# Performance work log

Measured on AMD Instinct MI355X. Metric: run time of the kernel, lower is better.

## Reference

```python
import jax, jax.numpy as jnp
import numpy as np


def setup_inputs() -> dict:
    key = jax.random.key(0)
    k1, k2 = jax.random.split(key)
    N, K, D = 65536, 512, 512
    x = jax.random.normal(k1, (N, D), dtype=jnp.float32)
    centroids = jax.random.normal(k2, (K, D), dtype=jnp.float32)
    return {"x": x, "centroids": centroids}


def reference(x, centroids):
    # Squared pairwise distances via matmul expansion (same math as
    # sum((x[:,None,:] - c[None,:,:])**2, axis=2), without the [N,K,D] blowup):
    x_sq = jnp.sum(x * x, axis=1, keepdims=True)            # [N, 1]
    c_sq = jnp.sum(centroids * centroids, axis=1)            # [K]
    d2 = x_sq + c_sq[None, :] - 2.0 * (x @ centroids.T)      # [N, K]
    q = 1.0 / (1.0 + d2)                                     # Student-t kernel, alpha=1
    q = q / jnp.sum(q, axis=1, keepdims=True)                # row normalize
    return q
```

## Files before the change

kernel.cpp:

```cpp
#include <hip/hip_runtime.h>
#include <stdint.h>


#define D 512
#define K 512
#define BM 64
#define BK 64
#define NCHUNK (D / BK)
#define THREADS 512

typedef __attribute__((ext_vector_type(8))) short short8;
typedef __attribute__((ext_vector_type(4))) float floatx4;

__device__ __forceinline__ uint16_t f2bf(float f) {
  uint32_t u = __float_as_uint(f);
  u += 0x7FFFu + ((u >> 16) & 1u);
  return (uint16_t)(u >> 16);
}

__global__ __launch_bounds__(64)
void prep_kernel(const float* __restrict__ cent, float* __restrict__ csq,
                 uint16_t* __restrict__ bbf) {
  const int row  = blockIdx.x;
  const int lane = threadIdx.x;
  const float4* src = (const float4*)(cent + (size_t)row * D + lane * 8);
  float4 v0 = src[0];
  float4 v1 = src[1];
  float ss = v0.x*v0.x + v0.y*v0.y + v0.z*v0.z + v0.w*v0.w
           + v1.x*v1.x + v1.y*v1.y + v1.z*v1.z + v1.w*v1.w;
  uint4 pk;
  pk.x = (uint32_t)f2bf(v0.x) | ((uint32_t)f2bf(v0.y) << 16);
  pk.y = (uint32_t)f2bf(v0.z) | ((uint32_t)f2bf(v0.w) << 16);
  pk.z = (uint32_t)f2bf(v1.x) | ((uint32_t)f2bf(v1.y) << 16);
  pk.w = (uint32_t)f2bf(v1.z) | ((uint32_t)f2bf(v1.w) << 16);
  const int c = lane >> 3;
  const int g = lane & 7;
  const int slot = (c * K + row) * 8 + (g ^ (row & 7));
  *(uint4*)(bbf + (size_t)slot * 8) = pk;
  #pragma unroll
  for (int m = 1; m < 64; m <<= 1) ss += __shfl_xor(ss, m);
  if (lane == 0) csq[row] = ss;
}

__global__ __launch_bounds__(THREADS, 4)
void cluster_main(const float* __restrict__ x, const uint16_t* __restrict__ bbf,
                  const float* __restrict__ csq, float* __restrict__ out) {
  __shared__ __align__(16) uint16_t lA[BM * BK];
  __shared__ __align__(16) uint16_t lB[K * BK];
  __shared__ float lcsq[K];
  __shared__ float lxsq[BM];
  __shared__ float lrow[BM];

  const int tid  = threadIdx.x;
  const int wave = tid >> 6;
  const int lane = tid & 63;
  const int p    = lane & 15;
  const int quad = lane >> 4;
  const int row0 = blockIdx.x * BM;

  lcsq[tid] = csq[tid];
  if (tid < BM) { lxsq[tid] = 0.f; lrow[tid] = 0.f; }

  const int ar = tid >> 3;
  const int ag = tid & 7;
  const float* aptr = x + (size_t)(row0 + ar) * D + ag * 8;
  uint16_t* adst = &lA[(size_t)(ar * 8 + (ag ^ (ar & 7))) * 8];
  float xacc = 0.f;

  floatx4 acc[4][4];
  #pragma unroll
  for (int mi = 0; mi < 4; ++mi)
    #pragma unroll
    for (int ni = 0; ni < 4; ++ni)
      acc[mi][ni] = (floatx4){0.f, 0.f, 0.f, 0.f};

  for (int c = 0; c < NCHUNK; ++c) {
    __syncthreads();

    float4 v0 = *(const float4*)(aptr);
    float4 v1 = *(const float4*)(aptr + 4);
    aptr += BK;
    xacc += v0.x*v0.x + v0.y*v0.y + v0.z*v0.z + v0.w*v0.w
          + v1.x*v1.x + v1.y*v1.y + v1.z*v1.z + v1.w*v1.w;
    uint4 pk;
    pk.x = (uint32_t)f2bf(v0.x) | ((uint32_t)f2bf(v0.y) << 16);
    pk.y = (uint32_t)f2bf(v0.z) | ((uint32_t)f2bf(v0.w) << 16);
    pk.z = (uint32_t)f2bf(v1.x) | ((uint32_t)f2bf(v1.y) << 16);
    pk.w = (uint32_t)f2bf(v1.z) | ((uint32_t)f2bf(v1.w) << 16);
    *(uint4*)adst = pk;

    {
      const uint16_t* bsrc = bbf + (size_t)c * (K * BK) + wave * 4096 + lane * 8;
      #pragma unroll
      for (int j = 0; j < 8; ++j) {
        __builtin_amdgcn_global_load_lds(
            (const __attribute__((address_space(1))) uint32_t*)(bsrc + j * 512),
            (__attribute__((address_space(3))) uint32_t*)(&lB[wave * 4096 + j * 512]),
            16, 0, 0);
      }
    }

    __syncthreads();

    #pragma unroll
    for (int kk = 0; kk < 2; ++kk) {
      short8 af[4], bfr[4];
      #pragma unroll
      for (int mi = 0; mi < 4; ++mi) {
        const int r = mi * 16 + p;
        const int g = (kk * 4 + quad) ^ (r & 7);
        af[mi] = *(const short8*)&lA[(size_t)(r * 8 + g) * 8];
      }
      #pragma unroll
      for (int ni = 0; ni < 4; ++ni) {
        const int r = wave * 64 + ni * 16 + p;
        const int g = (kk * 4 + quad) ^ (r & 7);
        bfr[ni] = *(const short8*)&lB[(size_t)(r * 8 + g) * 8];
      }
      #pragma unroll
      for (int mi = 0; mi < 4; ++mi)
        #pragma unroll
        for (int ni = 0; ni < 4; ++ni)
          acc[mi][ni] = __builtin_amdgcn_mfma_f32_16x16x32_bf16(
              af[mi], bfr[ni], acc[mi][ni], 0, 0, 0);
    }
  }

  atomicAdd(&lxsq[ar], xacc);
  __syncthreads();

  float xs[4][4];
  #pragma unroll
  for (int mi = 0; mi < 4; ++mi)
    #pragma unroll
    for (int rr = 0; rr < 4; ++rr)
      xs[mi][rr] = lxsq[mi * 16 + quad * 4 + rr];
  float cs[4];
  #pragma unroll
  for (int ni = 0; ni < 4; ++ni)
    cs[ni] = lcsq[wave * 64 + ni * 16 + p];

  float rp[4][4];
  #pragma unroll
  for (int mi = 0; mi < 4; ++mi)
    #pragma unroll
    for (int rr = 0; rr < 4; ++rr)
      rp[mi][rr] = 0.f;

  #pragma unroll
  for (int mi = 0; mi < 4; ++mi)
    #pragma unroll
    for (int ni = 0; ni < 4; ++ni)
      #pragma unroll
      for (int rr = 0; rr < 4; ++rr) {
        const float d = 1.0f + xs[mi][rr] + cs[ni] - 2.0f * acc[mi][ni][rr];
        const float q = __builtin_amdgcn_rcpf(d);
        acc[mi][ni][rr] = q;
        rp[mi][rr] += q;
      }

  #pragma unroll
  for (int mi = 0; mi < 4; ++mi)
    #pragma unroll
    for (int rr = 0; rr < 4; ++rr) {
      float v = rp[mi][rr];
      v += __shfl_xor(v, 1);
      v += __shfl_xor(v, 2);
      v += __shfl_xor(v, 4);
      v += __shfl_xor(v, 8);
      if (p == 0) atomicAdd(&lrow[mi * 16 + quad * 4 + rr], v);
    }
  __syncthreads();

  #pragma unroll
  for (int mi = 0; mi < 4; ++mi) {
    #pragma unroll
    for (int rr = 0; rr < 4; ++rr) {
      const int row = mi * 16 + quad * 4 + rr;
      const float inv = __builtin_amdgcn_rcpf(lrow[row]);
      float* orow = out + (size_t)(row0 + row) * K + wave * 64 + p;
      #pragma unroll
      for (int ni = 0; ni < 4; ++ni)
        orow[ni * 16] = acc[mi][ni][rr] * inv;
    }
  }
}

extern "C" void kernel_launch(void* const* d_in, const int* in_sizes, int n_in,
                              void* d_out, int out_size, void* d_ws, size_t ws_size,
                              hipStream_t stream) {
  const float* x    = (const float*)d_in[0];
  const float* cent = (const float*)d_in[1];
  float* out = (float*)d_out;

  float*    csq = (float*)d_ws;
  uint16_t* bbf = (uint16_t*)((char*)d_ws + 2048);

  const int N = in_sizes[0] / D;
  prep_kernel<<<K, 64, 0, stream>>>(cent, csq, bbf);
  cluster_main<<<N / BM, THREADS, 0, stream>>>(x, bbf, csq, out);
}
```

Baseline: 260.7 us.

## Double-buffer LDS tiles with halved K-chunk and register prefetch of x

```diff
diff --git a/kernel.cpp b/kernel.cpp
--- a/kernel.cpp
+++ b/kernel.cpp
@@ -5,7 +5,7 @@
 #define D 512
 #define K 512
 #define BM 64
-#define BK 64
+#define BK 32
 #define NCHUNK (D / BK)
 #define THREADS 512
 
@@ -16,6 +16,13 @@
   uint32_t u = __float_as_uint(f);
   u += 0x7FFFu + ((u >> 16) & 1u);
   return (uint16_t)(u >> 16);
+}
+
+__device__ __forceinline__ uint2 pack4(float4 v) {
+  uint2 p;
+  p.x = (uint32_t)f2bf(v.x) | ((uint32_t)f2bf(v.y) << 16);
+  p.y = (uint32_t)f2bf(v.z) | ((uint32_t)f2bf(v.w) << 16);
+  return p;
 }
 
 __global__ __launch_bounds__(64)
@@ -29,14 +36,11 @@
   float ss = v0.x*v0.x + v0.y*v0.y + v0.z*v0.z + v0.w*v0.w
            + v1.x*v1.x + v1.y*v1.y + v1.z*v1.z + v1.w*v1.w;
   uint4 pk;
-  pk.x = (uint32_t)f2bf(v0.x) | ((uint32_t)f2bf(v0.y) << 16);
-  pk.y = (uint32_t)f2bf(v0.z) | ((uint32_t)f2bf(v0.w) << 16);
-  pk.z = (uint32_t)f2bf(v1.x) | ((uint32_t)f2bf(v1.y) << 16);
-  pk.w = (uint32_t)f2bf(v1.z) | ((uint32_t)f2bf(v1.w) << 16);
-  const int c = lane >> 3;
-  const int g = lane & 7;
-  const int slot = (c * K + row) * 8 + (g ^ (row & 7));
-  *(uint4*)(bbf + (size_t)slot * 8) = pk;
+  { uint2 a = pack4(v0), b = pack4(v1); pk.x = a.x; pk.y = a.y; pk.z = b.x; pk.w = b.y; }
+  const int c = lane >> 2;
+  const int g = lane & 3;
+  const size_t eo = ((size_t)(c * K + row)) * 32 + (size_t)((g ^ ((row >> 2) & 3))) * 8;
+  *(uint4*)(bbf + eo) = pk;
   #pragma unroll
   for (int m = 1; m < 64; m <<= 1) ss += __shfl_xor(ss, m);
   if (lane == 0) csq[row] = ss;
@@ -45,8 +49,8 @@
 __global__ __launch_bounds__(THREADS, 4)
 void cluster_main(const float* __restrict__ x, const uint16_t* __restrict__ bbf,
                   const float* __restrict__ csq, float* __restrict__ out) {
-  __shared__ __align__(16) uint16_t lA[BM * BK];
-  __shared__ __align__(16) uint16_t lB[K * BK];
+  __shared__ __align__(16) uint16_t lA[2][BM * BK];
+  __shared__ __align__(16) uint16_t lB[2][K * BK];
   __shared__ float lcsq[K];
   __shared__ float lxsq[BM];
   __shared__ float lrow[BM];
@@ -56,16 +60,18 @@
   const int lane = tid & 63;
   const int p    = lane & 15;
   const int quad = lane >> 4;
+  const int sw   = quad ^ (p >> 2);
   const int row0 = blockIdx.x * BM;
 
   lcsq[tid] = csq[tid];
   if (tid < BM) { lxsq[tid] = 0.f; lrow[tid] = 0.f; }
 
-  const int ar = tid >> 3;
-  const int ag = tid & 7;
-  const float* aptr = x + (size_t)(row0 + ar) * D + ag * 8;
-  uint16_t* adst = &lA[(size_t)(ar * 8 + (ag ^ (ar & 7))) * 8];
-  float xacc = 0.f;
+  const int ar  = tid >> 3;
+  const int sub = tid & 7;
+  const int aidx = (ar * 4 + ((sub >> 1) ^ ((ar >> 2) & 3))) * 8 + (sub & 1) * 4;
+  const float* aptr = x + (size_t)(row0 + ar) * D + sub * 4;
+
+  const int bofs = wave * 2048 + lane * 8;
 
   floatx4 acc[4][4];
   #pragma unroll
@@ -74,55 +80,73 @@
     for (int ni = 0; ni < 4; ++ni)
       acc[mi][ni] = (floatx4){0.f, 0.f, 0.f, 0.f};
 
+  float xacc;
+  float4 areg;
+
+  {
+    const uint16_t* src = bbf + bofs;
+    uint16_t* dst = &lB[0][wave * 2048];
+    #pragma unroll
+    for (int j = 0; j < 4; ++j)
+      __builtin_amdgcn_global_load_lds(
+          (const __attribute__((address_space(1))) uint32_t*)(src + j * 512),
+          (__attribute__((address_space(3))) uint32_t*)(dst + j * 512),
+          16, 0, 0);
+    float4 a0 = *(const float4*)(aptr);
+    xacc = a0.x*a0.x + a0.y*a0.y + a0.z*a0.z + a0.w*a0.w;
+    *(uint2*)&lA[0][aidx] = pack4(a0);
+    areg = *(const float4*)(aptr + BK);
+  }
+  __syncthreads();
+  {
+    const uint16_t* src = bbf + (size_t)1 * (K * BK) + bofs;
+    uint16_t* dst = &lB[1][wave * 2048];
+    #pragma unroll
+    for (int j = 0; j < 4; ++j)
+      __builtin_amdgcn_global_load_lds(
+          (const __attribute__((address_space(1))) uint32_t*)(src + j * 512),
+          (__attribute__((address_space(3))) uint32_t*)(dst + j * 512),
+          16, 0, 0);
+  }
+
   for (int c = 0; c < NCHUNK; ++c) {
+    const int buf = c & 1;
+
+    if (c + 1 < NCHUNK) {
+      xacc += areg.x*areg.x + areg.y*areg.y + areg.z*areg.z + areg.w*areg.w;
+      *(uint2*)&lA[(c + 1) & 1][aidx] = pack4(areg);
+    }
+    if (c + 2 < NCHUNK) areg = *(const float4*)(aptr + (c + 2) * BK);
+
+    short8 af[4], bfr[4];
+    #pragma unroll
+    for (int mi = 0; mi < 4; ++mi) {
+      const int r = mi * 16 + p;
+      af[mi] = *(const short8*)&lA[buf][r * 32 + sw * 8];
+    }
+    #pragma unroll
+    for (int ni = 0; ni < 4; ++ni) {
+      const int r = wave * 64 + ni * 16 + p;
+      bfr[ni] = *(const short8*)&lB[buf][r * 32 + sw * 8];
+    }
+    #pragma unroll
+    for (int mi = 0; mi < 4; ++mi)
+      #pragma unroll
+      for (int ni = 0; ni < 4; ++ni)
+        acc[mi][ni] = __builtin_amdgcn_mfma_f32_16x16x32_bf16(
+            af[mi], bfr[ni], acc[mi][ni], 0, 0, 0);
+
     __syncthreads();
 
-    float4 v0 = *(const float4*)(aptr);
-    float4 v1 = *(const float4*)(aptr + 4);
-    aptr += BK;
-    xacc += v0.x*v0.x + v0.y*v0.y + v0.z*v0.z + v0.w*v0.w
-          + v1.x*v1.x + v1.y*v1.y + v1.z*v1.z + v1.w*v1.w;
-    uint4 pk;
-    pk.x = (uint32_t)f2bf(v0.x) | ((uint32_t)f2bf(v0.y) << 16);
-    pk.y = (uint32_t)f2bf(v0.z) | ((uint32_t)f2bf(v0.w) << 16);
-    pk.z = (uint32_t)f2bf(v1.x) | ((uint32_t)f2bf(v1.y) << 16);
-    pk.w = (uint32_t)f2bf(v1.z) | ((uint32_t)f2bf(v1.w) << 16);
-    *(uint4*)adst = pk;
-
-    {
-      const uint16_t* bsrc = bbf + (size_t)c * (K * BK) + wave * 4096 + lane * 8;
-      #pragma unroll
-      for (int j = 0; j < 8; ++j) {
+    if (c + 2 < NCHUNK) {
+      const uint16_t* src = bbf + (size_t)(c + 2) * (K * BK) + bofs;
+      uint16_t* dst = &lB[buf][wave * 2048];
+      #pragma unroll
+      for (int j = 0; j < 4; ++j)
         __builtin_amdgcn_global_load_lds(
-            (const __attribute__((address_space(1))) uint32_t*)(bsrc + j * 512),
-            (__attribute__((address_space(3))) uint32_t*)(&lB[wave * 4096 + j * 512]),
+            (const __attribute__((address_space(1))) uint32_t*)(src + j * 512),
+            (__attribute__((address_space(3))) uint32_t*)(dst + j * 512),
             16, 0, 0);
-      }
-    }
-
-    __syncthreads();
-
-    #pragma unroll
-    for (int kk = 0; kk < 2; ++kk) {
-      short8 af[4], bfr[4];
-      #pragma unroll
-      for (int mi = 0; mi < 4; ++mi) {
-        const int r = mi * 16 + p;
-        const int g = (kk * 4 + quad) ^ (r & 7);
-        af[mi] = *(const short8*)&lA[(size_t)(r * 8 + g) * 8];
-      }
-      #pragma unroll
-      for (int ni = 0; ni < 4; ++ni) {
-        const int r = wave * 64 + ni * 16 + p;
-        const int g = (kk * 4 + quad) ^ (r & 7);
-        bfr[ni] = *(const short8*)&lB[(size_t)(r * 8 + g) * 8];
-      }
-      #pragma unroll
-      for (int mi = 0; mi < 4; ++mi)
-        #pragma unroll
-        for (int ni = 0; ni < 4; ++ni)
-          acc[mi][ni] = __builtin_amdgcn_mfma_f32_16x16x32_bf16(
-              af[mi], bfr[ni], acc[mi][ni], 0, 0, 0);
     }
   }
 
```

New measurement: 273.3 us. 1.05x slower.
